# Kernel tuning notes

Hardware: AMD Instinct MI355X
Metric: run time of the kernel (lower is better)

Reference implementation:

```python
import jax, jax.numpy as jnp
import numpy as np

B, S, H, NH = 4, 2048, 1024, 16
D = H // NH

def setup_inputs() -> dict:
    key = jax.random.key(0)
    ks = jax.random.split(key, 9)
    sc = 1.0 / np.sqrt(H)
    return {
        "x": jax.random.normal(ks[0], (B, S, H), jnp.float32),
        "Wq": jax.random.normal(ks[1], (H, H), jnp.float32) * sc,
        "bq": jax.random.normal(ks[2], (H,), jnp.float32) * 0.01,
        "Wk": jax.random.normal(ks[3], (H, H), jnp.float32) * sc,
        "bk": jax.random.normal(ks[4], (H,), jnp.float32) * 0.01,
        "Wv": jax.random.normal(ks[5], (H, H), jnp.float32) * sc,
        "bv": jax.random.normal(ks[6], (H,), jnp.float32) * 0.01,
        "Wo": jax.random.normal(ks[7], (H, H), jnp.float32) * sc,
        "bo": jax.random.normal(ks[8], (H,), jnp.float32) * 0.01,
    }

def reference(x, Wq, bq, Wk, bk, Wv, bv, Wo, bo):
    # torch Linear: y = x @ W.T + b
    def proj(x, W, b):
        # [B,S,H] -> [B,NH,S,D]
        y = jnp.einsum('bsh,oh->bso', x, W) + b
        return y.reshape(B, S, NH, D).transpose(0, 2, 1, 3)
    q = proj(x, Wq, bq)
    k = proj(x, Wk, bk)
    v = proj(x, Wv, bv)
    scores = jnp.einsum('bhqd,bhkd->bhqk', q, k) / jnp.sqrt(jnp.float32(D))
    p = jax.nn.softmax(scores, axis=-1)  # [B,NH,S,S]
    o = jnp.einsum('bhqk,bhkd->bhqd', p, v)  # dropout p=0 (eval)
    o = o.transpose(0, 2, 1, 3).reshape(B, S, H)
    return jnp.einsum('bsh,oh->bso', o, Wo) + bo
```

## Files before the change

kernel.cpp:

```cpp
#include <hip/hip_runtime.h>


#define DEV __device__ __forceinline__

typedef __bf16 bf16x8 __attribute__((ext_vector_type(8)));
typedef __bf16 bf16x4 __attribute__((ext_vector_type(4)));
typedef __bf16 bf16x2 __attribute__((ext_vector_type(2)));
typedef float floatx4 __attribute__((ext_vector_type(4)));
typedef unsigned int uintx4 __attribute__((ext_vector_type(4)));

constexpr int Bdim = 4, SS = 2048, HH = 1024, NHH = 16, DD = 64;
constexpr int MM = Bdim * SS;

DEV void async16(const void* g, void* l) {
  __builtin_amdgcn_global_load_lds(
      (const __attribute__((address_space(1))) unsigned int*)g,
      (__attribute__((address_space(3))) unsigned int*)l, 16, 0, 0);
}

DEV int swz3(int r) { return (r ^ (r >> 3)) & 7; }

DEV unsigned pkbf16(float lo, float hi) {
  bf16x2 t;
  t[0] = (__bf16)lo;
  t[1] = (__bf16)hi;
  return __builtin_bit_cast(unsigned, t);
}

DEV void pswap16(unsigned& a, unsigned& b) {
  asm("v_permlane16_swap_b32 %0, %1" : "+v"(a), "+v"(b));
}

__global__ __launch_bounds__(256) void cast_bf16_kernel(
    const float* __restrict__ x, const float* __restrict__ wq,
    const float* __restrict__ wk, const float* __restrict__ wv,
    const float* __restrict__ wo,
    __bf16* __restrict__ xb, __bf16* __restrict__ wqb, __bf16* __restrict__ wkb,
    __bf16* __restrict__ wvb, __bf16* __restrict__ wob) {
  const float* src; __bf16* dst; int n4;
  switch (blockIdx.z) {
    case 0: src = x;  dst = xb;  n4 = MM * HH / 4; break;
    case 1: src = wq; dst = wqb; n4 = HH * HH / 4; break;
    case 2: src = wk; dst = wkb; n4 = HH * HH / 4; break;
    case 3: src = wv; dst = wvb; n4 = HH * HH / 4; break;
    default: src = wo; dst = wob; n4 = HH * HH / 4; break;
  }
  int stride = gridDim.x * blockDim.x;
  for (int i = blockIdx.x * blockDim.x + threadIdx.x; i < n4; i += stride) {
    float4 v = ((const float4*)src)[i];
    bf16x4 o;
    o[0] = (__bf16)v.x; o[1] = (__bf16)v.y; o[2] = (__bf16)v.z; o[3] = (__bf16)v.w;
    ((bf16x4*)dst)[i] = o;
  }
}

DEV void gemm8p(const __bf16* __restrict__ Ablk, const __bf16* __restrict__ Bblk,
                __bf16* Ab, __bf16* Bb, floatx4 acc[4][4]) {
  const int t = threadIdx.x;
  const int lane = t & 63, quad = lane >> 4, l16 = lane & 15;
  const int wid = t >> 6;
  const int wm = (wid >> 2) * 64, wn = (wid & 3) * 64;

  const int rl = t >> 3, ch = t & 7;
  const __bf16* Ag[2];
  Ag[0] = Ablk + (size_t)rl * HH + (ch ^ swz3(rl)) * 8;
  Ag[1] = Ablk + (size_t)(rl + 64) * HH + (ch ^ swz3(rl + 64)) * 8;
  const __bf16* Bg[4];
#pragma unroll
  for (int br = 0; br < 4; ++br)
    Bg[br] = Bblk + (size_t)(rl + 64 * br) * HH + (ch ^ swz3(rl + 64 * br)) * 8;

  int aoff[2][4], boff[2][4];
#pragma unroll
  for (int kk = 0; kk < 2; ++kk)
#pragma unroll
    for (int i = 0; i < 4; ++i) {
      int ra = wm + i * 16 + l16;
      aoff[kk][i] = ra * 64 + (((kk * 4 + quad) ^ swz3(ra)) * 8);
      int rb = wn + i * 16 + l16;
      boff[kk][i] = rb * 64 + (((kk * 4 + quad) ^ swz3(rb)) * 8);
    }

#pragma unroll
  for (int tile = 0; tile < 2; ++tile) {
    async16(Ag[0] + tile * 64, Ab + tile * 8192 + t * 8);
    async16(Ag[1] + tile * 64, Ab + tile * 8192 + 4096 + t * 8);
#pragma unroll
    for (int br = 0; br < 4; ++br)
      async16(Bg[br] + tile * 64, Bb + tile * 16384 + br * 4096 + t * 8);
  }
  asm volatile("s_waitcnt vmcnt(0)" ::: "memory");
  __builtin_amdgcn_s_barrier();

  int cb = 0, sb = 2;
#pragma unroll 1
  for (int kt = 0; kt < 16; ++kt) {
    const __bf16* Ac = Ab + cb * 8192;
    const __bf16* Bc = Bb + cb * 16384;
    __bf16* Asg = Ab + sb * 8192;
    __bf16* Bsg = Bb + sb * 16384;
    const int ks = (kt + 2) * 64;
    const bool st = kt < 14;

    bf16x8 af[4], bfr[4];
#pragma unroll
    for (int i = 0; i < 4; ++i) af[i] = *(const bf16x8*)&Ac[aoff[0][i]];
#pragma unroll
    for (int i = 0; i < 4; ++i) bfr[i] = *(const bf16x8*)&Bc[boff[0][i]];
    if (st) {
      async16(Ag[0] + ks, Asg + t * 8);
      async16(Ag[1] + ks, Asg + 4096 + t * 8);
      async16(Bg[0] + ks, Bsg + t * 8);
    }
    asm volatile("" ::: "memory");
    __builtin_amdgcn_s_barrier();
    asm volatile("s_waitcnt lgkmcnt(0)" ::: "memory");
    __builtin_amdgcn_sched_barrier(0);
    __builtin_amdgcn_s_setprio(1);
#pragma unroll
    for (int mi = 0; mi < 4; ++mi)
#pragma unroll
      for (int ni = 0; ni < 4; ++ni)
        acc[mi][ni] = __builtin_amdgcn_mfma_f32_16x16x32_bf16(af[mi], bfr[ni],
                                                              acc[mi][ni], 0, 0, 0);
    __builtin_amdgcn_s_setprio(0);
    asm volatile("" ::: "memory");
    __builtin_amdgcn_s_barrier();

#pragma unroll
    for (int i = 0; i < 4; ++i) af[i] = *(const bf16x8*)&Ac[aoff[1][i]];
#pragma unroll
    for (int i = 0; i < 4; ++i) bfr[i] = *(const bf16x8*)&Bc[boff[1][i]];
    if (st) {
      async16(Bg[1] + ks, Bsg + 4096 + t * 8);
      async16(Bg[2] + ks, Bsg + 8192 + t * 8);
      async16(Bg[3] + ks, Bsg + 12288 + t * 8);
    }
    asm volatile("" ::: "memory");
    __builtin_amdgcn_s_barrier();
    asm volatile("s_waitcnt lgkmcnt(0)" ::: "memory");
    __builtin_amdgcn_sched_barrier(0);
    __builtin_amdgcn_s_setprio(1);
#pragma unroll
    for (int mi = 0; mi < 4; ++mi)
#pragma unroll
      for (int ni = 0; ni < 4; ++ni)
        acc[mi][ni] = __builtin_amdgcn_mfma_f32_16x16x32_bf16(af[mi], bfr[ni],
                                                              acc[mi][ni], 0, 0, 0);
    __builtin_amdgcn_s_setprio(0);
    if (st) asm volatile("s_waitcnt vmcnt(6)" ::: "memory");
    else    asm volatile("s_waitcnt vmcnt(0)" ::: "memory");
    asm volatile("" ::: "memory");
    __builtin_amdgcn_s_barrier();

    cb = cb == 2 ? 0 : cb + 1;
    sb = sb == 2 ? 0 : sb + 1;
  }
}

__global__ __launch_bounds__(512, 2) void proj_qkv_kernel(
    const __bf16* __restrict__ xb,
    const __bf16* __restrict__ wqb, const __bf16* __restrict__ wkb,
    const __bf16* __restrict__ wvb,
    const float* __restrict__ bq, const float* __restrict__ bk,
    const float* __restrict__ bv,
    __bf16* __restrict__ Q, __bf16* __restrict__ Kc, __bf16* __restrict__ Vt) {
  __shared__ __align__(16) __bf16 Ab[3][128 * 64];
  __shared__ __align__(16) __bf16 Bb[3][256 * 64];

  const int lid = blockIdx.x;
  const int xcd = lid & 7, slot = lid >> 3;
  const int mp = xcd + 8 * (slot & 7);
  const int nt = slot >> 3;
  const int mode = nt >> 2;
  const int n0 = (nt & 3) * 256;
  const int m0 = mp * 128;

  const __bf16* W = mode == 0 ? wqb : mode == 1 ? wkb : wvb;
  const float* bias = mode == 0 ? bq : mode == 1 ? bk : bv;

  floatx4 acc[4][4] = {};
  gemm8p(xb + (size_t)m0 * HH, W + (size_t)n0 * HH, &Ab[0][0], &Bb[0][0], acc);

  const int t = threadIdx.x, lane = t & 63, quad = lane >> 4, l16 = lane & 15;
  const int wid = t >> 6, wm = (wid >> 2) * 64, wn = (wid & 3) * 64;
  const float qscale = 0.125f * 1.44269504088896f;

#pragma unroll
  for (int ni = 0; ni < 4; ++ni) {
    int n = n0 + wn + ni * 16 + l16;
    float bval = bias[n];
    int h = n >> 6, d = n & 63;
#pragma unroll
    for (int mi = 0; mi < 4; ++mi) {
      int mbase = m0 + wm + mi * 16 + quad * 4;
      int bb = mbase >> 11, sbase = mbase & (SS - 1);
      size_t bh = (size_t)(bb * NHH + h);
      if (mode == 2) {
        bf16x4 pv;
#pragma unroll
        for (int r = 0; r < 4; ++r) pv[r] = (__bf16)(acc[mi][ni][r] + bval);
        *(bf16x4*)&Vt[(bh * DD + d) * SS + sbase] = pv;
      } else {
#pragma unroll
        for (int r = 0; r < 4; ++r) {
          float v = acc[mi][ni][r] + bval;
          if (mode == 0) Q [(bh * SS + sbase + r) * DD + d] = (__bf16)(v * qscale);
          else           Kc[(bh * SS + sbase + r) * DD + d] = (__bf16)v;
        }
      }
    }
  }
}

__global__ __launch_bounds__(512, 2) void proj_out_kernel(
    const __bf16* __restrict__ Ob, const __bf16* __restrict__ wob,
    const float* __restrict__ bo, float* __restrict__ out) {
  __shared__ __align__(16) __bf16 Ab[3][128 * 64];
  __shared__ __align__(16) __bf16 Bb[3][256 * 64];

  const int lid = blockIdx.x;
  const int xcd = lid & 7, slot = lid >> 3;
  const int mp = xcd + 8 * (slot & 7);
  const int np = slot >> 3;
  const int m0 = mp * 128, n0 = np * 256;

  floatx4 acc[4][4] = {};
  gemm8p(Ob + (size_t)m0 * HH, wob + (size_t)n0 * HH, &Ab[0][0], &Bb[0][0], acc);

  const int t = threadIdx.x, lane = t & 63, quad = lane >> 4, l16 = lane & 15;
  const int wid = t >> 6, wm = (wid >> 2) * 64, wn = (wid & 3) * 64;
#pragma unroll
  for (int ni = 0; ni < 4; ++ni) {
    int n = n0 + wn + ni * 16 + l16;
    float bval = bo[n];
#pragma unroll
    for (int mi = 0; mi < 4; ++mi)
#pragma unroll
      for (int r = 0; r < 4; ++r) {
        int m = m0 + wm + mi * 16 + quad * 4 + r;
        out[(size_t)m * HH + n] = acc[mi][ni][r] + bval;
      }
  }
}

__global__ __launch_bounds__(256, 2) void attn_kernel(
    const __bf16* __restrict__ Q, const __bf16* __restrict__ Kc,
    const __bf16* __restrict__ Vt, __bf16* __restrict__ Ob) {
  __shared__ __align__(16) __bf16 Ks[2][64 * 64];
  __shared__ __align__(16) __bf16 Vs[2][64 * 64];

  const int t = threadIdx.x, lane = t & 63, quad = lane >> 4, l16 = lane & 15;
  const int wid = t >> 6;
  const int L = blockIdx.x;
  const int qt = L >> 6, bhx = L & 63;
  const int b = bhx >> 4, h = bhx & 15;
  const size_t bh = (size_t)b * NHH + h;
  const __bf16* Qg = Q + (bh * SS + (size_t)qt * 256) * DD;
  const __bf16* Kg = Kc + bh * SS * DD;
  const __bf16* Vg = Vt + bh * DD * SS;

  const int srow = t >> 3;
  const int sc = t & 7;

  const __bf16* KgA = Kg + (size_t)srow * DD + (sc ^ swz3(srow)) * 8;
  const __bf16* KgB = Kg + (size_t)(srow + 32) * DD + (sc ^ swz3(srow + 32)) * 8;
  const __bf16* VgA = Vg + (size_t)srow * SS + (sc ^ swz3(srow)) * 8;
  const __bf16* VgB = Vg + (size_t)(srow + 32) * SS + (sc ^ swz3(srow + 32)) * 8;

  bf16x8 qf[4][2];
#pragma unroll
  for (int ni = 0; ni < 4; ++ni)
#pragma unroll
    for (int ks = 0; ks < 2; ++ks)
      qf[ni][ks] = *(const bf16x8*)(Qg + (size_t)(wid * 64 + ni * 16 + l16) * DD
                                    + (ks * 4 + quad) * 8);

  floatx4 oacc[4][4] = {};
  floatx4 rsacc[4] = {};
  const floatx4 z4 = {0.f, 0.f, 0.f, 0.f};
  bf16x8 ones;
#pragma unroll
  for (int i = 0; i < 8; ++i) ones[i] = (__bf16)1.0f;

  int koff[4][2];
#pragma unroll
  for (int mi = 0; mi < 4; ++mi) {
    int r = mi * 16 + l16;
#pragma unroll
    for (int ks = 0; ks < 2; ++ks)
      koff[mi][ks] = r * 64 + ((ks * 4 + quad) ^ swz3(r)) * 8;
  }
  const int sq = ((quad & 1) << 1) | (quad >> 1);
  int voff[4][2];
#pragma unroll
  for (int nj = 0; nj < 4; ++nj) {
    int r = nj * 16 + l16;
#pragma unroll
    for (int hf = 0; hf < 2; ++hf)
      voff[nj][hf] = r * 64 + ((hf * 4 + sq) ^ swz3(r)) * 8;
  }

  async16(KgA, &Ks[0][t * 8]);
  async16(KgB, &Ks[0][2048 + t * 8]);
  async16(VgA, &Vs[0][t * 8]);
  async16(VgB, &Vs[0][2048 + t * 8]);

  for (int kt = 0; kt < SS / 64; ++kt) {
    const int cur = kt & 1;
    __syncthreads();

    if (kt + 1 < SS / 64) {
      const int kk = (kt + 1) * 64;
      const int nxt = cur ^ 1;
      async16(KgA + (size_t)kk * DD, &Ks[nxt][t * 8]);
      async16(KgB + (size_t)kk * DD, &Ks[nxt][2048 + t * 8]);
      async16(VgA + kk, &Vs[nxt][t * 8]);
      async16(VgB + kk, &Vs[nxt][2048 + t * 8]);
    }

    floatx4 sacc[4][4];
    {
      bf16x8 kf[4];
#pragma unroll
      for (int mi = 0; mi < 4; ++mi) kf[mi] = *(const bf16x8*)&Ks[cur][koff[mi][0]];
#pragma unroll
      for (int mi = 0; mi < 4; ++mi)
#pragma unroll
        for (int ni = 0; ni < 4; ++ni)
          sacc[mi][ni] = __builtin_amdgcn_mfma_f32_16x16x32_bf16(kf[mi], qf[ni][0],
                                                                 z4, 0, 0, 0);
#pragma unroll
      for (int mi = 0; mi < 4; ++mi) kf[mi] = *(const bf16x8*)&Ks[cur][koff[mi][1]];
#pragma unroll
      for (int mi = 0; mi < 4; ++mi)
#pragma unroll
        for (int ni = 0; ni < 4; ++ni)
          sacc[mi][ni] = __builtin_amdgcn_mfma_f32_16x16x32_bf16(kf[mi], qf[ni][1],
                                                                 sacc[mi][ni], 0, 0, 0);
    }

#pragma unroll
    for (int hf = 0; hf < 2; ++hf) {
      bf16x8 ap[4], bv8[4];
#pragma unroll
      for (int mq = 0; mq < 4; ++mq) {
        float p[2][4];
#pragma unroll
        for (int m = 0; m < 2; ++m)
#pragma unroll
          for (int r = 0; r < 4; ++r)
            p[m][r] = __builtin_amdgcn_exp2f(sacc[hf * 2 + m][mq][r]);
        unsigned x0 = pkbf16(p[0][0], p[0][1]);
        unsigned x1 = pkbf16(p[0][2], p[0][3]);
        unsigned y0 = pkbf16(p[1][0], p[1][1]);
        unsigned y1 = pkbf16(p[1][2], p[1][3]);
        pswap16(x0, y0);
        pswap16(x1, y1);
        uintx4 u = {x0, x1, y0, y1};
        ap[mq] = __builtin_bit_cast(bf16x8, u);
      }
#pragma unroll
      for (int nj = 0; nj < 4; ++nj) bv8[nj] = *(const bf16x8*)&Vs[cur][voff[nj][hf]];
#pragma unroll
      for (int mq = 0; mq < 4; ++mq) {
#pragma unroll
        for (int nj = 0; nj < 4; ++nj)
          oacc[mq][nj] = __builtin_amdgcn_mfma_f32_16x16x32_bf16(ap[mq], bv8[nj],
                                                                 oacc[mq][nj], 0, 0, 0);
        rsacc[mq] = __builtin_amdgcn_mfma_f32_16x16x32_bf16(ap[mq], ones,
                                                            rsacc[mq], 0, 0, 0);
      }
    }
  }

  const int s0 = qt * 256 + wid * 64;
#pragma unroll
  for (int mq = 0; mq < 4; ++mq) {
#pragma unroll
    for (int r = 0; r < 4; ++r) {
      float inv = 1.f / rsacc[mq][r];
      int s = s0 + mq * 16 + quad * 4 + r;
#pragma unroll
      for (int nj = 0; nj < 4; ++nj) {
        int d = nj * 16 + l16;
        Ob[((size_t)b * SS + s) * HH + h * DD + d] = (__bf16)(oacc[mq][nj][r] * inv);
      }
    }
  }
}

extern "C" void kernel_launch(void* const* d_in, const int* in_sizes, int n_in,
                              void* d_out, int out_size, void* d_ws, size_t ws_size,
                              hipStream_t stream) {
  const float* x  = (const float*)d_in[0];
  const float* Wq = (const float*)d_in[1];
  const float* bq = (const float*)d_in[2];
  const float* Wk = (const float*)d_in[3];
  const float* bk = (const float*)d_in[4];
  const float* Wv = (const float*)d_in[5];
  const float* bv = (const float*)d_in[6];
  const float* Wo = (const float*)d_in[7];
  const float* bo = (const float*)d_in[8];
  float* out = (float*)d_out;

  char* ws = (char*)d_ws;
  __bf16* xb  = (__bf16*)(ws);
  __bf16* wqb = (__bf16*)(ws + 16777216);
  __bf16* wkb = (__bf16*)(ws + 18874368);
  __bf16* wvb = (__bf16*)(ws + 20971520);
  __bf16* wob = (__bf16*)(ws + 23068672);
  __bf16* Qb  = (__bf16*)(ws + 25165824);
  __bf16* Kb  = (__bf16*)(ws + 41943040);
  __bf16* Vtb = (__bf16*)(ws + 58720256);
  __bf16* Ob  = (__bf16*)(ws + 75497472);

  cast_bf16_kernel<<<dim3(256, 1, 5), 256, 0, stream>>>(x, Wq, Wk, Wv, Wo,
                                                        xb, wqb, wkb, wvb, wob);
  proj_qkv_kernel<<<dim3(768), 512, 0, stream>>>(xb, wqb, wkb, wvb,
                                                 bq, bk, bv, Qb, Kb, Vtb);
  attn_kernel<<<dim3(512), 256, 0, stream>>>(Qb, Kb, Vtb, Ob);
  proj_out_kernel<<<dim3(256), 512, 0, stream>>>(Ob, wob, bo, out);
}
```

Measured before the change: 270.8 us.

## Enlarge GEMM block tile to 256x256 with double-buffered LDS pipeline

The projection GEMMs now use a 256x256 output tile per 512-thread block (each wave computes 128x64) instead of 128x256, halving the grid sizes. The LDS pipeline drops from triple to double buffering, now prefetching one k-tile ahead with a full vmcnt(0) wait each iteration. The aim is more arithmetic per loaded byte and fewer redundant A/B loads. In exchange it uses more accumulator registers, has a shallower prefetch, and launches only 128 blocks for the output projection, which may underfill the GPU.

```diff
diff --git a/kernel.cpp b/kernel.cpp
--- a/kernel.cpp
+++ b/kernel.cpp
@@ -54,63 +54,59 @@
   }
 }
 
-DEV void gemm8p(const __bf16* __restrict__ Ablk, const __bf16* __restrict__ Bblk,
-                __bf16* Ab, __bf16* Bb, floatx4 acc[4][4]) {
+DEV void gemm256(const __bf16* __restrict__ Ablk, const __bf16* __restrict__ Bblk,
+                 __bf16* Ab, __bf16* Bb, floatx4 acc[8][4]) {
   const int t = threadIdx.x;
   const int lane = t & 63, quad = lane >> 4, l16 = lane & 15;
   const int wid = t >> 6;
-  const int wm = (wid >> 2) * 64, wn = (wid & 3) * 64;
+  const int wm = (wid >> 2) * 128, wn = (wid & 3) * 64;
 
   const int rl = t >> 3, ch = t & 7;
-  const __bf16* Ag[2];
-  Ag[0] = Ablk + (size_t)rl * HH + (ch ^ swz3(rl)) * 8;
-  Ag[1] = Ablk + (size_t)(rl + 64) * HH + (ch ^ swz3(rl + 64)) * 8;
+  const __bf16* Ag[4];
   const __bf16* Bg[4];
 #pragma unroll
-  for (int br = 0; br < 4; ++br)
-    Bg[br] = Bblk + (size_t)(rl + 64 * br) * HH + (ch ^ swz3(rl + 64 * br)) * 8;
-
-  int aoff[2][4], boff[2][4];
-#pragma unroll
-  for (int kk = 0; kk < 2; ++kk)
-#pragma unroll
-    for (int i = 0; i < 4; ++i) {
-      int ra = wm + i * 16 + l16;
-      aoff[kk][i] = ra * 64 + (((kk * 4 + quad) ^ swz3(ra)) * 8);
-      int rb = wn + i * 16 + l16;
-      boff[kk][i] = rb * 64 + (((kk * 4 + quad) ^ swz3(rb)) * 8);
-    }
-
-#pragma unroll
-  for (int tile = 0; tile < 2; ++tile) {
-    async16(Ag[0] + tile * 64, Ab + tile * 8192 + t * 8);
-    async16(Ag[1] + tile * 64, Ab + tile * 8192 + 4096 + t * 8);
-#pragma unroll
-    for (int br = 0; br < 4; ++br)
-      async16(Bg[br] + tile * 64, Bb + tile * 16384 + br * 4096 + t * 8);
-  }
+  for (int r = 0; r < 4; ++r) {
+    Ag[r] = Ablk + (size_t)(rl + 64 * r) * HH + (ch ^ swz3(rl + 64 * r)) * 8;
+    Bg[r] = Bblk + (size_t)(rl + 64 * r) * HH + (ch ^ swz3(rl + 64 * r)) * 8;
+  }
+
+  int aoff[8], boff[4];
+#pragma unroll
+  for (int i = 0; i < 8; ++i) {
+    int ra = wm + i * 16 + l16;
+    aoff[i] = ra * 64 + ((quad ^ swz3(ra)) * 8);
+  }
+#pragma unroll
+  for (int j = 0; j < 4; ++j) {
+    int rb = wn + j * 16 + l16;
+    boff[j] = rb * 64 + ((quad ^ swz3(rb)) * 8);
+  }
+
+#pragma unroll
+  for (int r = 0; r < 4; ++r) async16(Ag[r], Ab + r * 4096 + t * 8);
+#pragma unroll
+  for (int r = 0; r < 4; ++r) async16(Bg[r], Bb + r * 4096 + t * 8);
   asm volatile("s_waitcnt vmcnt(0)" ::: "memory");
   __builtin_amdgcn_s_barrier();
 
-  int cb = 0, sb = 2;
 #pragma unroll 1
   for (int kt = 0; kt < 16; ++kt) {
-    const __bf16* Ac = Ab + cb * 8192;
+    const int cb = kt & 1;
+    const __bf16* Ac = Ab + cb * 16384;
     const __bf16* Bc = Bb + cb * 16384;
-    __bf16* Asg = Ab + sb * 8192;
-    __bf16* Bsg = Bb + sb * 16384;
-    const int ks = (kt + 2) * 64;
-    const bool st = kt < 14;
-
-    bf16x8 af[4], bfr[4];
-#pragma unroll
-    for (int i = 0; i < 4; ++i) af[i] = *(const bf16x8*)&Ac[aoff[0][i]];
-#pragma unroll
-    for (int i = 0; i < 4; ++i) bfr[i] = *(const bf16x8*)&Bc[boff[0][i]];
+    __bf16* Asg = Ab + (cb ^ 1) * 16384;
+    __bf16* Bsg = Bb + (cb ^ 1) * 16384;
+    const int ks = (kt + 1) * 64;
+    const bool st = kt < 15;
+
+    bf16x8 af[8], bfr[4];
+#pragma unroll
+    for (int i = 0; i < 8; ++i) af[i] = *(const bf16x8*)&Ac[aoff[i]];
+#pragma unroll
+    for (int j = 0; j < 4; ++j) bfr[j] = *(const bf16x8*)&Bc[boff[j]];
     if (st) {
-      async16(Ag[0] + ks, Asg + t * 8);
-      async16(Ag[1] + ks, Asg + 4096 + t * 8);
-      async16(Bg[0] + ks, Bsg + t * 8);
+#pragma unroll
+      for (int r = 0; r < 4; ++r) async16(Ag[r] + ks, Asg + r * 4096 + t * 8);
     }
     asm volatile("" ::: "memory");
     __builtin_amdgcn_s_barrier();
@@ -118,7 +114,7 @@
     __builtin_amdgcn_sched_barrier(0);
     __builtin_amdgcn_s_setprio(1);
 #pragma unroll
-    for (int mi = 0; mi < 4; ++mi)
+    for (int mi = 0; mi < 8; ++mi)
 #pragma unroll
       for (int ni = 0; ni < 4; ++ni)
         acc[mi][ni] = __builtin_amdgcn_mfma_f32_16x16x32_bf16(af[mi], bfr[ni],
@@ -128,13 +124,12 @@
     __builtin_amdgcn_s_barrier();
 
 #pragma unroll
-    for (int i = 0; i < 4; ++i) af[i] = *(const bf16x8*)&Ac[aoff[1][i]];
-#pragma unroll
-    for (int i = 0; i < 4; ++i) bfr[i] = *(const bf16x8*)&Bc[boff[1][i]];
+    for (int i = 0; i < 8; ++i) af[i] = *(const bf16x8*)&Ac[aoff[i] ^ 32];
+#pragma unroll
+    for (int j = 0; j < 4; ++j) bfr[j] = *(const bf16x8*)&Bc[boff[j] ^ 32];
     if (st) {
-      async16(Bg[1] + ks, Bsg + 4096 + t * 8);
-      async16(Bg[2] + ks, Bsg + 8192 + t * 8);
-      async16(Bg[3] + ks, Bsg + 12288 + t * 8);
+#pragma unroll
+      for (int r = 0; r < 4; ++r) async16(Bg[r] + ks, Bsg + r * 4096 + t * 8);
     }
     asm volatile("" ::: "memory");
     __builtin_amdgcn_s_barrier();
@@ -142,19 +137,15 @@
     __builtin_amdgcn_sched_barrier(0);
     __builtin_amdgcn_s_setprio(1);
 #pragma unroll
-    for (int mi = 0; mi < 4; ++mi)
+    for (int mi = 0; mi < 8; ++mi)
 #pragma unroll
       for (int ni = 0; ni < 4; ++ni)
         acc[mi][ni] = __builtin_amdgcn_mfma_f32_16x16x32_bf16(af[mi], bfr[ni],
                                                               acc[mi][ni], 0, 0, 0);
     __builtin_amdgcn_s_setprio(0);
-    if (st) asm volatile("s_waitcnt vmcnt(6)" ::: "memory");
-    else    asm volatile("s_waitcnt vmcnt(0)" ::: "memory");
+    asm volatile("s_waitcnt vmcnt(0)" ::: "memory");
     asm volatile("" ::: "memory");
     __builtin_amdgcn_s_barrier();
-
-    cb = cb == 2 ? 0 : cb + 1;
-    sb = sb == 2 ? 0 : sb + 1;
   }
 }
 
@@ -165,25 +156,25 @@
     const float* __restrict__ bq, const float* __restrict__ bk,
     const float* __restrict__ bv,
     __bf16* __restrict__ Q, __bf16* __restrict__ Kc, __bf16* __restrict__ Vt) {
-  __shared__ __align__(16) __bf16 Ab[3][128 * 64];
-  __shared__ __align__(16) __bf16 Bb[3][256 * 64];
+  __shared__ __align__(16) __bf16 Ab[2][256 * 64];
+  __shared__ __align__(16) __bf16 Bb[2][256 * 64];
 
   const int lid = blockIdx.x;
   const int xcd = lid & 7, slot = lid >> 3;
-  const int mp = xcd + 8 * (slot & 7);
-  const int nt = slot >> 3;
+  const int mp = xcd + 8 * (slot & 3);
+  const int nt = slot >> 2;
   const int mode = nt >> 2;
   const int n0 = (nt & 3) * 256;
-  const int m0 = mp * 128;
+  const int m0 = mp * 256;
 
   const __bf16* W = mode == 0 ? wqb : mode == 1 ? wkb : wvb;
   const float* bias = mode == 0 ? bq : mode == 1 ? bk : bv;
 
-  floatx4 acc[4][4] = {};
-  gemm8p(xb + (size_t)m0 * HH, W + (size_t)n0 * HH, &Ab[0][0], &Bb[0][0], acc);
+  floatx4 acc[8][4] = {};
+  gemm256(xb + (size_t)m0 * HH, W + (size_t)n0 * HH, &Ab[0][0], &Bb[0][0], acc);
 
   const int t = threadIdx.x, lane = t & 63, quad = lane >> 4, l16 = lane & 15;
-  const int wid = t >> 6, wm = (wid >> 2) * 64, wn = (wid & 3) * 64;
+  const int wid = t >> 6, wm = (wid >> 2) * 128, wn = (wid & 3) * 64;
   const float qscale = 0.125f * 1.44269504088896f;
 
 #pragma unroll
@@ -192,7 +183,7 @@
     float bval = bias[n];
     int h = n >> 6, d = n & 63;
 #pragma unroll
-    for (int mi = 0; mi < 4; ++mi) {
+    for (int mi = 0; mi < 8; ++mi) {
       int mbase = m0 + wm + mi * 16 + quad * 4;
       int bb = mbase >> 11, sbase = mbase & (SS - 1);
       size_t bh = (size_t)(bb * NHH + h);
@@ -216,26 +207,26 @@
 __global__ __launch_bounds__(512, 2) void proj_out_kernel(
     const __bf16* __restrict__ Ob, const __bf16* __restrict__ wob,
     const float* __restrict__ bo, float* __restrict__ out) {
-  __shared__ __align__(16) __bf16 Ab[3][128 * 64];
-  __shared__ __align__(16) __bf16 Bb[3][256 * 64];
+  __shared__ __align__(16) __bf16 Ab[2][256 * 64];
+  __shared__ __align__(16) __bf16 Bb[2][256 * 64];
 
   const int lid = blockIdx.x;
   const int xcd = lid & 7, slot = lid >> 3;
-  const int mp = xcd + 8 * (slot & 7);
-  const int np = slot >> 3;
-  const int m0 = mp * 128, n0 = np * 256;
-
-  floatx4 acc[4][4] = {};
-  gemm8p(Ob + (size_t)m0 * HH, wob + (size_t)n0 * HH, &Ab[0][0], &Bb[0][0], acc);
+  const int mp = xcd + 8 * (slot & 3);
+  const int np = slot >> 2;
+  const int m0 = mp * 256, n0 = np * 256;
+
+  floatx4 acc[8][4] = {};
+  gemm256(Ob + (size_t)m0 * HH, wob + (size_t)n0 * HH, &Ab[0][0], &Bb[0][0], acc);
 
   const int t = threadIdx.x, lane = t & 63, quad = lane >> 4, l16 = lane & 15;
-  const int wid = t >> 6, wm = (wid >> 2) * 64, wn = (wid & 3) * 64;
+  const int wid = t >> 6, wm = (wid >> 2) * 128, wn = (wid & 3) * 64;
 #pragma unroll
   for (int ni = 0; ni < 4; ++ni) {
     int n = n0 + wn + ni * 16 + l16;
     float bval = bo[n];
 #pragma unroll
-    for (int mi = 0; mi < 4; ++mi)
+    for (int mi = 0; mi < 8; ++mi)
 #pragma unroll
       for (int r = 0; r < 4; ++r) {
         int m = m0 + wm + mi * 16 + quad * 4 + r;
@@ -417,8 +408,8 @@
 
   cast_bf16_kernel<<<dim3(256, 1, 5), 256, 0, stream>>>(x, Wq, Wk, Wv, Wo,
                                                         xb, wqb, wkb, wvb, wob);
-  proj_qkv_kernel<<<dim3(768), 512, 0, stream>>>(xb, wqb, wkb, wvb,
+  proj_qkv_kernel<<<dim3(384), 512, 0, stream>>>(xb, wqb, wkb, wvb,
                                                  bq, bk, bv, Qb, Kb, Vtb);
   attn_kernel<<<dim3(512), 256, 0, stream>>>(Qb, Kb, Vtb, Ob);
-  proj_out_kernel<<<dim3(256), 512, 0, stream>>>(Ob, wob, bo, out);
-}
+  proj_out_kernel<<<dim3(128), 512, 0, stream>>>(Ob, wob, bo, out);
+}
```

After: 290.3 us. +7.2%, slower.
